# Performance work log

Hardware: AMD Instinct MI355X
Metric: run time of the kernel (lower is better)

Reference implementation:

```python
import jax, jax.numpy as jnp
import numpy as np

BATCH_SIZE = 4
TEMPERATURE = 0.07
NEG_MASK_VAL = -10.0


def setup_inputs() -> dict:
    key = jax.random.key(0)
    k1, k2 = jax.random.split(key)
    N, D = 16384, 256  # N = batch_size * n_patches
    feat_q = jax.random.normal(k1, (N, D), dtype=jnp.float32)
    feat_k = jax.random.normal(k2, (N, D), dtype=jnp.float32)
    return {"feat_q": feat_q, "feat_k": feat_k}


def reference(feat_q, feat_k):
    N, d = feat_q.shape
    feat_k = jax.lax.stop_gradient(feat_k)  # detach
    # positive logits: dot of matching rows -> [N, 1]
    l_pos = jnp.einsum('nd,nd->n', feat_q, feat_k)[:, None]
    q = feat_q.reshape(BATCH_SIZE, -1, d)  # [B, P, D]
    k = feat_k.reshape(BATCH_SIZE, -1, d)
    P = q.shape[1]
    # intra-batch-element negatives: [B, P, P]
    l_neg = jnp.einsum('bpd,bqd->bpq', q, k)
    eye = jnp.eye(P, dtype=bool)[None, :, :]
    l_neg = jnp.where(eye, jnp.float32(NEG_MASK_VAL), l_neg).reshape(-1, P)
    out = jnp.concatenate([l_pos, l_neg], axis=1) / TEMPERATURE  # [N, 1+P]
    # cross-entropy with target class 0, reduction='none'
    loss = -jax.nn.log_softmax(out, axis=1)[:, 0]
    return loss
```

## Files before the change

### kernel.cpp

```cpp
#include <hip/hip_runtime.h>
#include <hip/hip_bf16.h>


typedef __attribute__((ext_vector_type(8))) short short8;
typedef __attribute__((ext_vector_type(4))) float f32x4;

#define BATCH 4
#define PN 4096
#define DD 256
#define NP (BATCH * PN)

constexpr float kLog2e = 1.4426950408889634f;
constexpr float kScale = kLog2e / 0.07f;
constexpr float kMask2 = -10.0f * kScale;
constexpr float kLn2   = 0.6931471805599453f;
constexpr float kNegInf = -3.0e38f;

__device__ __forceinline__ unsigned short f2bf(float f) {
  __hip_bfloat16 h = __float2bfloat16(f);
  return *reinterpret_cast<unsigned short*>(&h);
}

__device__ __forceinline__ float fexp2(float x) {
#if __has_builtin(__builtin_amdgcn_exp2f)
  return __builtin_amdgcn_exp2f(x);
#else
  return exp2f(x);
#endif
}
__device__ __forceinline__ float flog2(float x) {
#if __has_builtin(__builtin_amdgcn_logf)
  return __builtin_amdgcn_logf(x);
#else
  return log2f(x);
#endif
}

__global__ void k_convert(const float* __restrict__ src,
                          unsigned short* __restrict__ dst, int n4) {
  int i = blockIdx.x * blockDim.x + threadIdx.x;
  if (i >= n4) return;
  float4 v = reinterpret_cast<const float4*>(src)[i];
  ushort4 o;
  o.x = f2bf(v.x); o.y = f2bf(v.y); o.z = f2bf(v.z); o.w = f2bf(v.w);
  reinterpret_cast<ushort4*>(dst)[i] = o;
}

__device__ __forceinline__ void stage16(const char* __restrict__ src,
                                        char* ldsbase, int tid) {
  const int wv = tid >> 6;
#pragma unroll
  for (int ip = 0; ip < 4; ip++) {
    const int o   = ip * 4096 + tid * 16;
    const int row = o >> 9;
    const int so  = o ^ ((row & 15) << 4);
    __builtin_amdgcn_global_load_lds(
        (const __attribute__((address_space(1))) void*)(src + so),
        (__attribute__((address_space(3))) void*)(ldsbase + ip * 4096 + wv * 1024),
        16, 0, 0);
  }
}

__device__ __forceinline__ void stage_tile(const char* __restrict__ src,
                                           char* ldsbase, int tid) {
  const int wv = tid >> 6;
#pragma unroll
  for (int ip = 0; ip < 8; ip++) {
    const int o   = ip * 4096 + tid * 16;
    const int row = o >> 9;
    const int so  = o ^ ((row & 15) << 4);
    __builtin_amdgcn_global_load_lds(
        (const __attribute__((address_space(1))) void*)(src + so),
        (__attribute__((address_space(3))) void*)(ldsbase + ip * 4096 + wv * 1024),
        16, 0, 0);
  }
}

__global__ __launch_bounds__(256)
__attribute__((amdgpu_waves_per_eu(2, 2)))
void k_nce256(const float* __restrict__ fq, const unsigned short* __restrict__ kb,
              float* __restrict__ pl, float* __restrict__ pp) {
  __shared__ __align__(16) char kt[2][32 * 512];

  const int blk = blockIdx.x;
  const int b   = blk & 3;
  const int r2  = blk >> 2;
  const int rt  = r2 & 15;
  const int kc  = r2 >> 4;
  const int R0  = rt * 256;
  const int C0  = kc * 512;
  const int tid = threadIdx.x;
  const int w   = tid >> 6;
  const int l   = tid & 63;
  const int g   = l >> 4;
  const int li  = l & 15;

  const char* ksrc = reinterpret_cast<const char*>(kb) +
                     ((size_t)b * PN + C0) * 512;

  stage16(ksrc, kt[0], tid);

  short8 a[4][8];
#pragma unroll
  for (int af = 0; af < 4; af++) {
    const float* qrow =
        fq + ((size_t)(b * PN + R0 + w * 64 + af * 16 + li)) * DD;
#pragma unroll
    for (int ks = 0; ks < 8; ks++) {
      const float* p = qrow + ks * 32 + g * 8;
      float4 v0 = *reinterpret_cast<const float4*>(p);
      float4 v1 = *reinterpret_cast<const float4*>(p + 4);
      a[af][ks][0] = (short)f2bf(v0.x * kScale);
      a[af][ks][1] = (short)f2bf(v0.y * kScale);
      a[af][ks][2] = (short)f2bf(v0.z * kScale);
      a[af][ks][3] = (short)f2bf(v0.w * kScale);
      a[af][ks][4] = (short)f2bf(v1.x * kScale);
      a[af][ks][5] = (short)f2bf(v1.y * kScale);
      a[af][ks][6] = (short)f2bf(v1.z * kScale);
      a[af][ks][7] = (short)f2bf(v1.w * kScale);
    }
  }

  float m[4][4], lsum[4][4];
#pragma unroll
  for (int af = 0; af < 4; af++)
#pragma unroll
    for (int r = 0; r < 4; r++) { m[af][r] = kNegInf; lsum[af][r] = 0.f; }

  __syncthreads();

  for (int ct = 0; ct < 16; ct++) {
    const int cur = ct & 1;
    if (ct + 1 < 16) stage16(ksrc + (size_t)(ct + 1) * 16384, kt[cur ^ 1], tid);

    const char* lb = kt[cur];
    f32x4 acc[4][2];
#pragma unroll
    for (int af = 0; af < 4; af++)
#pragma unroll
      for (int cf = 0; cf < 2; cf++) acc[af][cf] = f32x4{0.f, 0.f, 0.f, 0.f};

#pragma unroll
    for (int ks = 0; ks < 8; ks++) {
#pragma unroll
      for (int cf = 0; cf < 2; cf++) {
        const int row = cf * 16 + li;
        const int off = row * 512 + ((ks * 64 + g * 16) ^ ((row & 15) << 4));
        short8 bf = *reinterpret_cast<const short8*>(lb + off);
#pragma unroll
        for (int af = 0; af < 4; af++)
          acc[af][cf] = __builtin_amdgcn_mfma_f32_16x16x32_bf16(a[af][ks], bf,
                                                                acc[af][cf], 0, 0, 0);
      }
    }

#pragma unroll
    for (int af = 0; af < 4; af++) {
      const int G = rt * 16 + w * 4 + af;
      if ((G >> 5) == kc && ct == ((G >> 1) - kc * 16)) {
        if ((G & 1) == 0) {
#pragma unroll
          for (int r = 0; r < 4; r++)
            if (li == g * 4 + r) {
              pp[b * PN + R0 + w * 64 + af * 16 + g * 4 + r] = acc[af][0][r];
              acc[af][0][r] = kMask2;
            }
        } else {
#pragma unroll
          for (int r = 0; r < 4; r++)
            if (li == g * 4 + r) {
              pp[b * PN + R0 + w * 64 + af * 16 + g * 4 + r] = acc[af][1][r];
              acc[af][1][r] = kMask2;
            }
        }
      }
    }

#pragma unroll
    for (int af = 0; af < 4; af++)
#pragma unroll
      for (int r = 0; r < 4; r++) {
        float v0 = acc[af][0][r], v1 = acc[af][1][r];
        float t0 = fmaxf(v0, v1);
        float mo = m[af][r];
        float mn = fmaxf(mo, t0);
        lsum[af][r] = lsum[af][r] * fexp2(mo - mn) + fexp2(v0 - mn) + fexp2(v1 - mn);
        m[af][r] = mn;
      }
    __syncthreads();
  }

#pragma unroll
  for (int af = 0; af < 4; af++)
#pragma unroll
    for (int r = 0; r < 4; r++) {
      float m_ = m[af][r], l_ = lsum[af][r];
#pragma unroll
      for (int off = 1; off < 16; off <<= 1) {
        float mo = __shfl_xor(m_, off, 64);
        float lo = __shfl_xor(l_, off, 64);
        float mn = fmaxf(m_, mo);
        l_ = l_ * fexp2(m_ - mn) + lo * fexp2(mo - mn);
        m_ = mn;
      }
      if (li == 0) {
        const int rowg = b * PN + R0 + w * 64 + af * 16 + g * 4 + r;
        pl[kc * NP + rowg] = m_ + flog2(l_);
      }
    }
}

template <int NC>
__global__ void k_combine(const float* __restrict__ pl,
                          const float* __restrict__ pp,
                          float* __restrict__ out) {
  const int i = blockIdx.x * blockDim.x + threadIdx.x;
  if (i >= NP) return;
  float mm = kNegInf;
  float v[NC];
#pragma unroll
  for (int c = 0; c < NC; c++) { v[c] = pl[c * NP + i]; mm = fmaxf(mm, v[c]); }
  float s = 0.f;
#pragma unroll
  for (int c = 0; c < NC; c++) s += fexp2(v[c] - mm);
  float lse = mm + flog2(s);
  float p = pp[i];
  float mn = fmaxf(lse, p);
  float la = mn + flog2(fexp2(lse - mn) + fexp2(p - mn));
  out[i] = (la - p) * kLn2;
}

__global__ __launch_bounds__(256, 4) void k_nce32(
    const float* __restrict__ fq, const unsigned short* __restrict__ kb,
    float* __restrict__ pl, float* __restrict__ pp) {
  __shared__ __align__(16) char kt[2][32 * 512];

  const int blk = blockIdx.x;
  const int b   = blk & 3;
  const int rt  = (blk >> 2) & 31;
  const int kc  = blk >> 7;
  const int R0  = rt * 128;
  const int C0  = kc * 512;
  const int tid = threadIdx.x;
  const int w   = tid >> 6;
  const int l   = tid & 63;
  const int g   = l >> 4;
  const int li  = l & 15;

  const char* ksrc = reinterpret_cast<const char*>(kb) +
                     ((size_t)b * PN + C0) * 512;
  stage16(ksrc, kt[0], tid);

  short8 a[2][8];
#pragma unroll
  for (int af = 0; af < 2; af++) {
    const float* qrow = fq + ((size_t)(b * PN + R0 + w * 32 + af * 16 + li)) * DD;
#pragma unroll
    for (int ks = 0; ks < 8; ks++) {
      const float* p = qrow + ks * 32 + g * 8;
      float4 v0 = *reinterpret_cast<const float4*>(p);
      float4 v1 = *reinterpret_cast<const float4*>(p + 4);
      a[af][ks][0] = (short)f2bf(v0.x * kScale); a[af][ks][1] = (short)f2bf(v0.y * kScale);
      a[af][ks][2] = (short)f2bf(v0.z * kScale); a[af][ks][3] = (short)f2bf(v0.w * kScale);
      a[af][ks][4] = (short)f2bf(v1.x * kScale); a[af][ks][5] = (short)f2bf(v1.y * kScale);
      a[af][ks][6] = (short)f2bf(v1.z * kScale); a[af][ks][7] = (short)f2bf(v1.w * kScale);
    }
  }

  float m[2][4], lsum[2][4];
#pragma unroll
  for (int af = 0; af < 2; af++)
#pragma unroll
    for (int r = 0; r < 4; r++) { m[af][r] = kNegInf; lsum[af][r] = 0.f; }

  const int ctd = (kc == (rt >> 2)) ? ((rt & 3) * 4 + w) : -1;
  __syncthreads();

  for (int ct = 0; ct < 16; ct++) {
    const int cur = ct & 1;
    if (ct + 1 < 16) stage16(ksrc + (size_t)(ct + 1) * 16384, kt[cur ^ 1], tid);

    const char* lb = kt[cur];
    f32x4 acc[2][2];
#pragma unroll
    for (int af = 0; af < 2; af++)
#pragma unroll
      for (int cf = 0; cf < 2; cf++) acc[af][cf] = f32x4{0.f, 0.f, 0.f, 0.f};

#pragma unroll
    for (int ks = 0; ks < 8; ks++) {
#pragma unroll
      for (int cf = 0; cf < 2; cf++) {
        const int row = cf * 16 + li;
        const int off = row * 512 + ((ks * 64 + g * 16) ^ ((row & 15) << 4));
        short8 bf = *reinterpret_cast<const short8*>(lb + off);
        acc[0][cf] = __builtin_amdgcn_mfma_f32_16x16x32_bf16(a[0][ks], bf, acc[0][cf], 0, 0, 0);
        acc[1][cf] = __builtin_amdgcn_mfma_f32_16x16x32_bf16(a[1][ks], bf, acc[1][cf], 0, 0, 0);
      }
    }

    if (ct == ctd) {
#pragma unroll
      for (int af = 0; af < 2; af++)
#pragma unroll
        for (int r = 0; r < 4; r++)
          if (li == g * 4 + r) {
            pp[b * PN + R0 + w * 32 + af * 16 + g * 4 + r] = acc[af][af][r];
            acc[af][af][r] = kMask2;
          }
    }

#pragma unroll
    for (int af = 0; af < 2; af++)
#pragma unroll
      for (int r = 0; r < 4; r++) {
        float v0 = acc[af][0][r], v1 = acc[af][1][r];
        float t0 = fmaxf(v0, v1);
        float mo = m[af][r];
        float mn = fmaxf(mo, t0);
        lsum[af][r] = lsum[af][r] * fexp2(mo - mn) + fexp2(v0 - mn) + fexp2(v1 - mn);
        m[af][r] = mn;
      }
    __syncthreads();
  }

#pragma unroll
  for (int af = 0; af < 2; af++)
#pragma unroll
    for (int r = 0; r < 4; r++) {
      float m_ = m[af][r], l_ = lsum[af][r];
#pragma unroll
      for (int off = 1; off < 16; off <<= 1) {
        float mo = __shfl_xor(m_, off, 64);
        float lo = __shfl_xor(l_, off, 64);
        float mn = fmaxf(m_, mo);
        l_ = l_ * fexp2(m_ - mn) + lo * fexp2(mo - mn);
        m_ = mn;
      }
      if (li == 0) {
        const int rowg = b * PN + R0 + w * 32 + af * 16 + g * 4 + r;
        pl[kc * NP + rowg] = m_ + flog2(l_);
      }
    }
}

__global__ __launch_bounds__(256) void k_nce_full(const float* __restrict__ fq,
                                                  const unsigned short* __restrict__ kb,
                                                  float* __restrict__ out) {
  __shared__ __align__(16) char kt[2][64 * 512];
  const int blk = blockIdx.x;
  const int b = blk & 3, rt = blk >> 2;
  const int R0 = rt * 64;
  const int tid = threadIdx.x;
  const int w = tid >> 6, l = tid & 63, g = l >> 4, li = l & 15;

  const float* qrow = fq + ((size_t)(b * PN + R0 + w * 16 + li)) * DD;
  short8 a[8];
#pragma unroll
  for (int ks = 0; ks < 8; ks++) {
    const float* p = qrow + ks * 32 + g * 8;
    float4 v0 = *reinterpret_cast<const float4*>(p);
    float4 v1 = *reinterpret_cast<const float4*>(p + 4);
    a[ks][0] = (short)f2bf(v0.x * kScale); a[ks][1] = (short)f2bf(v0.y * kScale);
    a[ks][2] = (short)f2bf(v0.z * kScale); a[ks][3] = (short)f2bf(v0.w * kScale);
    a[ks][4] = (short)f2bf(v1.x * kScale); a[ks][5] = (short)f2bf(v1.y * kScale);
    a[ks][6] = (short)f2bf(v1.z * kScale); a[ks][7] = (short)f2bf(v1.w * kScale);
  }
  float m[4], lsum[4], pos[4];
#pragma unroll
  for (int r = 0; r < 4; r++) { m[r] = kNegInf; lsum[r] = 0.f; pos[r] = kNegInf; }
  const char* ksrc = reinterpret_cast<const char*>(kb + (size_t)b * PN * DD);
  stage_tile(ksrc, kt[0], tid);
  __syncthreads();
  for (int ct = 0; ct < 64; ct++) {
    const int cur = ct & 1;
    if (ct + 1 < 64) stage_tile(ksrc + (size_t)(ct + 1) * 32768, kt[cur ^ 1], tid);
    const char* lb = kt[cur];
    f32x4 acc[4];
#pragma unroll
    for (int cf = 0; cf < 4; cf++) acc[cf] = f32x4{0.f, 0.f, 0.f, 0.f};
#pragma unroll
    for (int ks = 0; ks < 8; ks++) {
#pragma unroll
      for (int cf = 0; cf < 4; cf++) {
        const int row = cf * 16 + li;
        const int off = row * 512 + ((ks * 64 + g * 16) ^ ((row & 15) << 4));
        short8 bf = *reinterpret_cast<const short8*>(lb + off);
        acc[cf] = __builtin_amdgcn_mfma_f32_16x16x32_bf16(a[ks], bf, acc[cf], 0, 0, 0);
      }
    }
    if (ct == rt) {
#pragma unroll
      for (int cf = 0; cf < 4; cf++)
        if (cf == w) {
#pragma unroll
          for (int r = 0; r < 4; r++)
            if (li == g * 4 + r) { pos[r] = acc[cf][r]; acc[cf][r] = kMask2; }
        }
    }
#pragma unroll
    for (int r = 0; r < 4; r++) {
      float t0 = fmaxf(fmaxf(acc[0][r], acc[1][r]), fmaxf(acc[2][r], acc[3][r]));
      float mo = m[r];
      float mn = fmaxf(mo, t0);
      float s = fexp2(acc[0][r] - mn) + fexp2(acc[1][r] - mn) +
                fexp2(acc[2][r] - mn) + fexp2(acc[3][r] - mn);
      lsum[r] = lsum[r] * fexp2(mo - mn) + s;
      m[r] = mn;
    }
    __syncthreads();
  }
#pragma unroll
  for (int r = 0; r < 4; r++) {
    float m_ = m[r], l_ = lsum[r], p_ = pos[r];
#pragma unroll
    for (int off = 1; off < 16; off <<= 1) {
      float mo = __shfl_xor(m_, off, 64);
      float lo = __shfl_xor(l_, off, 64);
      float po = __shfl_xor(p_, off, 64);
      float mn = fmaxf(m_, mo);
      l_ = l_ * fexp2(m_ - mn) + lo * fexp2(mo - mn);
      m_ = mn;
      p_ = fmaxf(p_, po);
    }
    float mn  = fmaxf(m_, p_);
    float lse = mn + flog2(l_ * fexp2(m_ - mn) + fexp2(p_ - mn));
    if (li == 0) out[b * PN + R0 + w * 16 + g * 4 + r] = (lse - p_) * kLn2;
  }
}

extern "C" void kernel_launch(void* const* d_in, const int* in_sizes, int n_in,
                              void* d_out, int out_size, void* d_ws, size_t ws_size,
                              hipStream_t stream) {
  const float* fq = (const float*)d_in[0];
  const float* fk = (const float*)d_in[1];
  float* out = (float*)d_out;
  unsigned short* kb = (unsigned short*)d_ws;
  const size_t kbBytes = (size_t)NP * DD * 2;
  const size_t ppBytes = (size_t)NP * 4;
  const size_t pl8Bytes = (size_t)8 * NP * 4;

  const int n4 = (NP * DD) / 4;
  hipLaunchKernelGGL(k_convert, dim3(n4 / 256), dim3(256), 0, stream, fk, kb, n4);

  if (ws_size >= kbBytes + pl8Bytes + ppBytes) {
    float* pl = (float*)((char*)d_ws + kbBytes);
    float* pp = (float*)((char*)d_ws + kbBytes + pl8Bytes);
    hipLaunchKernelGGL(k_nce256, dim3(512), dim3(256), 0, stream, fq, kb, pl, pp);
    hipLaunchKernelGGL(k_combine<8>, dim3(NP / 256), dim3(256), 0, stream, pl, pp, out);
  } else {
    hipLaunchKernelGGL(k_nce_full, dim3(BATCH * (PN / 64)), dim3(256), 0, stream,
                       fq, kb, out);
  }
}
```

Baseline: 63.50 us.

## Pre-convert Q to scaled bf16 and use smaller 128-row tiles with higher occupancy

A combined conversion kernel now turns both Q (pre-scaled) and K into bf16 in one launch. The main kernel becomes k_nceQ: 128-row tiles over 1024 blocks with 4 waves per EU, and it loads bf16 Q fragments directly instead of converting fp32 in registers. This removes the per-block fp32 Q reads and conversion, and aims for more parallelism and occupancy. In exchange it needs extra workspace and write traffic for the Q buffer, and each K tile is reused by fewer query rows.

```diff
diff --git a/kernel.cpp b/kernel.cpp
--- a/kernel.cpp
+++ b/kernel.cpp
@@ -34,6 +34,27 @@
 #else
   return log2f(x);
 #endif
+}
+
+__global__ void k_convert2(const float* __restrict__ fq,
+                           const float* __restrict__ fk,
+                           unsigned short* __restrict__ qb,
+                           unsigned short* __restrict__ kb, int n4each) {
+  int i = blockIdx.x * blockDim.x + threadIdx.x;
+  if (i < n4each) {
+    float4 v = reinterpret_cast<const float4*>(fq)[i];
+    ushort4 o;
+    o.x = f2bf(v.x * kScale); o.y = f2bf(v.y * kScale);
+    o.z = f2bf(v.z * kScale); o.w = f2bf(v.w * kScale);
+    reinterpret_cast<ushort4*>(qb)[i] = o;
+  } else {
+    int j = i - n4each;
+    if (j >= n4each) return;
+    float4 v = reinterpret_cast<const float4*>(fk)[j];
+    ushort4 o;
+    o.x = f2bf(v.x); o.y = f2bf(v.y); o.z = f2bf(v.z); o.w = f2bf(v.w);
+    reinterpret_cast<ushort4*>(kb)[j] = o;
+  }
 }
 
 __global__ void k_convert(const float* __restrict__ src,
@@ -77,162 +98,10 @@
 }
 
 __global__ __launch_bounds__(256)
-__attribute__((amdgpu_waves_per_eu(2, 2)))
-void k_nce256(const float* __restrict__ fq, const unsigned short* __restrict__ kb,
-              float* __restrict__ pl, float* __restrict__ pp) {
-  __shared__ __align__(16) char kt[2][32 * 512];
-
-  const int blk = blockIdx.x;
-  const int b   = blk & 3;
-  const int r2  = blk >> 2;
-  const int rt  = r2 & 15;
-  const int kc  = r2 >> 4;
-  const int R0  = rt * 256;
-  const int C0  = kc * 512;
-  const int tid = threadIdx.x;
-  const int w   = tid >> 6;
-  const int l   = tid & 63;
-  const int g   = l >> 4;
-  const int li  = l & 15;
-
-  const char* ksrc = reinterpret_cast<const char*>(kb) +
-                     ((size_t)b * PN + C0) * 512;
-
-  stage16(ksrc, kt[0], tid);
-
-  short8 a[4][8];
-#pragma unroll
-  for (int af = 0; af < 4; af++) {
-    const float* qrow =
-        fq + ((size_t)(b * PN + R0 + w * 64 + af * 16 + li)) * DD;
-#pragma unroll
-    for (int ks = 0; ks < 8; ks++) {
-      const float* p = qrow + ks * 32 + g * 8;
-      float4 v0 = *reinterpret_cast<const float4*>(p);
-      float4 v1 = *reinterpret_cast<const float4*>(p + 4);
-      a[af][ks][0] = (short)f2bf(v0.x * kScale);
-      a[af][ks][1] = (short)f2bf(v0.y * kScale);
-      a[af][ks][2] = (short)f2bf(v0.z * kScale);
-      a[af][ks][3] = (short)f2bf(v0.w * kScale);
-      a[af][ks][4] = (short)f2bf(v1.x * kScale);
-      a[af][ks][5] = (short)f2bf(v1.y * kScale);
-      a[af][ks][6] = (short)f2bf(v1.z * kScale);
-      a[af][ks][7] = (short)f2bf(v1.w * kScale);
-    }
-  }
-
-  float m[4][4], lsum[4][4];
-#pragma unroll
-  for (int af = 0; af < 4; af++)
-#pragma unroll
-    for (int r = 0; r < 4; r++) { m[af][r] = kNegInf; lsum[af][r] = 0.f; }
-
-  __syncthreads();
-
-  for (int ct = 0; ct < 16; ct++) {
-    const int cur = ct & 1;
-    if (ct + 1 < 16) stage16(ksrc + (size_t)(ct + 1) * 16384, kt[cur ^ 1], tid);
-
-    const char* lb = kt[cur];
-    f32x4 acc[4][2];
-#pragma unroll
-    for (int af = 0; af < 4; af++)
-#pragma unroll
-      for (int cf = 0; cf < 2; cf++) acc[af][cf] = f32x4{0.f, 0.f, 0.f, 0.f};
-
-#pragma unroll
-    for (int ks = 0; ks < 8; ks++) {
-#pragma unroll
-      for (int cf = 0; cf < 2; cf++) {
-        const int row = cf * 16 + li;
-        const int off = row * 512 + ((ks * 64 + g * 16) ^ ((row & 15) << 4));
-        short8 bf = *reinterpret_cast<const short8*>(lb + off);
-#pragma unroll
-        for (int af = 0; af < 4; af++)
-          acc[af][cf] = __builtin_amdgcn_mfma_f32_16x16x32_bf16(a[af][ks], bf,
-                                                                acc[af][cf], 0, 0, 0);
-      }
-    }
-
-#pragma unroll
-    for (int af = 0; af < 4; af++) {
-      const int G = rt * 16 + w * 4 + af;
-      if ((G >> 5) == kc && ct == ((G >> 1) - kc * 16)) {
-        if ((G & 1) == 0) {
-#pragma unroll
-          for (int r = 0; r < 4; r++)
-            if (li == g * 4 + r) {
-              pp[b * PN + R0 + w * 64 + af * 16 + g * 4 + r] = acc[af][0][r];
-              acc[af][0][r] = kMask2;
-            }
-        } else {
-#pragma unroll
-          for (int r = 0; r < 4; r++)
-            if (li == g * 4 + r) {
-              pp[b * PN + R0 + w * 64 + af * 16 + g * 4 + r] = acc[af][1][r];
-              acc[af][1][r] = kMask2;
-            }
-        }
-      }
-    }
-
-#pragma unroll
-    for (int af = 0; af < 4; af++)
-#pragma unroll
-      for (int r = 0; r < 4; r++) {
-        float v0 = acc[af][0][r], v1 = acc[af][1][r];
-        float t0 = fmaxf(v0, v1);
-        float mo = m[af][r];
-        float mn = fmaxf(mo, t0);
-        lsum[af][r] = lsum[af][r] * fexp2(mo - mn) + fexp2(v0 - mn) + fexp2(v1 - mn);
-        m[af][r] = mn;
-      }
-    __syncthreads();
-  }
-
-#pragma unroll
-  for (int af = 0; af < 4; af++)
-#pragma unroll
-    for (int r = 0; r < 4; r++) {
-      float m_ = m[af][r], l_ = lsum[af][r];
-#pragma unroll
-      for (int off = 1; off < 16; off <<= 1) {
-        float mo = __shfl_xor(m_, off, 64);
-        float lo = __shfl_xor(l_, off, 64);
-        float mn = fmaxf(m_, mo);
-        l_ = l_ * fexp2(m_ - mn) + lo * fexp2(mo - mn);
-        m_ = mn;
-      }
-      if (li == 0) {
-        const int rowg = b * PN + R0 + w * 64 + af * 16 + g * 4 + r;
-        pl[kc * NP + rowg] = m_ + flog2(l_);
-      }
-    }
-}
-
-template <int NC>
-__global__ void k_combine(const float* __restrict__ pl,
-                          const float* __restrict__ pp,
-                          float* __restrict__ out) {
-  const int i = blockIdx.x * blockDim.x + threadIdx.x;
-  if (i >= NP) return;
-  float mm = kNegInf;
-  float v[NC];
-#pragma unroll
-  for (int c = 0; c < NC; c++) { v[c] = pl[c * NP + i]; mm = fmaxf(mm, v[c]); }
-  float s = 0.f;
-#pragma unroll
-  for (int c = 0; c < NC; c++) s += fexp2(v[c] - mm);
-  float lse = mm + flog2(s);
-  float p = pp[i];
-  float mn = fmaxf(lse, p);
-  float la = mn + flog2(fexp2(lse - mn) + fexp2(p - mn));
-  out[i] = (la - p) * kLn2;
-}
-
-__global__ __launch_bounds__(256, 4) void k_nce32(
-    const float* __restrict__ fq, const unsigned short* __restrict__ kb,
-    float* __restrict__ pl, float* __restrict__ pp) {
+__attribute__((amdgpu_waves_per_eu(4, 4)))
+void k_nceQ(const unsigned short* __restrict__ qb,
+            const unsigned short* __restrict__ kb,
+            float* __restrict__ pl, float* __restrict__ pp) {
   __shared__ __align__(16) char kt[2][32 * 512];
 
   const int blk = blockIdx.x;
@@ -249,6 +118,143 @@
 
   const char* ksrc = reinterpret_cast<const char*>(kb) +
                      ((size_t)b * PN + C0) * 512;
+
+  stage16(ksrc, kt[0], tid);
+
+  short8 a[2][8];
+#pragma unroll
+  for (int af = 0; af < 2; af++) {
+    const unsigned short* qrow =
+        qb + (size_t)(b * PN + R0 + w * 32 + af * 16 + li) * DD;
+#pragma unroll
+    for (int ks = 0; ks < 8; ks++)
+      a[af][ks] = *reinterpret_cast<const short8*>(qrow + ks * 32 + g * 8);
+  }
+#pragma unroll
+  for (int af = 0; af < 2; af++)
+#pragma unroll
+    for (int ks = 0; ks < 8; ks++)
+      asm volatile("" : "+v"(a[af][ks]));
+
+  float m[2][4], lsum[2][4];
+#pragma unroll
+  for (int af = 0; af < 2; af++)
+#pragma unroll
+    for (int r = 0; r < 4; r++) { m[af][r] = kNegInf; lsum[af][r] = 0.f; }
+
+  const int ctd = (kc == (rt >> 2)) ? ((rt & 3) * 4 + w) : -1;
+
+  __syncthreads();
+
+  for (int ct = 0; ct < 16; ct++) {
+    const int cur = ct & 1;
+    if (ct + 1 < 16) stage16(ksrc + (size_t)(ct + 1) * 16384, kt[cur ^ 1], tid);
+
+    const char* lb = kt[cur];
+    f32x4 acc[2][2];
+#pragma unroll
+    for (int af = 0; af < 2; af++)
+#pragma unroll
+      for (int cf = 0; cf < 2; cf++) acc[af][cf] = f32x4{0.f, 0.f, 0.f, 0.f};
+
+#pragma unroll
+    for (int ks = 0; ks < 8; ks++) {
+#pragma unroll
+      for (int cf = 0; cf < 2; cf++) {
+        const int row = cf * 16 + li;
+        const int off = row * 512 + ((ks * 64 + g * 16) ^ ((row & 15) << 4));
+        short8 bf = *reinterpret_cast<const short8*>(lb + off);
+        acc[0][cf] = __builtin_amdgcn_mfma_f32_16x16x32_bf16(a[0][ks], bf,
+                                                             acc[0][cf], 0, 0, 0);
+        acc[1][cf] = __builtin_amdgcn_mfma_f32_16x16x32_bf16(a[1][ks], bf,
+                                                             acc[1][cf], 0, 0, 0);
+      }
+    }
+
+    if (ct == ctd) {
+#pragma unroll
+      for (int af = 0; af < 2; af++)
+#pragma unroll
+        for (int r = 0; r < 4; r++)
+          if (li == g * 4 + r) {
+            pp[b * PN + R0 + w * 32 + af * 16 + g * 4 + r] = acc[af][af][r];
+            acc[af][af][r] = kMask2;
+          }
+    }
+
+#pragma unroll
+    for (int af = 0; af < 2; af++)
+#pragma unroll
+      for (int r = 0; r < 4; r++) {
+        float v0 = acc[af][0][r], v1 = acc[af][1][r];
+        float t0 = fmaxf(v0, v1);
+        float mo = m[af][r];
+        float mn = fmaxf(mo, t0);
+        lsum[af][r] = lsum[af][r] * fexp2(mo - mn) + fexp2(v0 - mn) + fexp2(v1 - mn);
+        m[af][r] = mn;
+      }
+    __syncthreads();
+  }
+
+#pragma unroll
+  for (int af = 0; af < 2; af++)
+#pragma unroll
+    for (int r = 0; r < 4; r++) {
+      float m_ = m[af][r], l_ = lsum[af][r];
+#pragma unroll
+      for (int off = 1; off < 16; off <<= 1) {
+        float mo = __shfl_xor(m_, off, 64);
+        float lo = __shfl_xor(l_, off, 64);
+        float mn = fmaxf(m_, mo);
+        l_ = l_ * fexp2(m_ - mn) + lo * fexp2(mo - mn);
+        m_ = mn;
+      }
+      if (li == 0) {
+        const int rowg = b * PN + R0 + w * 32 + af * 16 + g * 4 + r;
+        pl[kc * NP + rowg] = m_ + flog2(l_);
+      }
+    }
+}
+
+template <int NC>
+__global__ void k_combine(const float* __restrict__ pl,
+                          const float* __restrict__ pp,
+                          float* __restrict__ out) {
+  const int i = blockIdx.x * blockDim.x + threadIdx.x;
+  if (i >= NP) return;
+  float mm = kNegInf;
+  float v[NC];
+#pragma unroll
+  for (int c = 0; c < NC; c++) { v[c] = pl[c * NP + i]; mm = fmaxf(mm, v[c]); }
+  float s = 0.f;
+#pragma unroll
+  for (int c = 0; c < NC; c++) s += fexp2(v[c] - mm);
+  float lse = mm + flog2(s);
+  float p = pp[i];
+  float mn = fmaxf(lse, p);
+  float la = mn + flog2(fexp2(lse - mn) + fexp2(p - mn));
+  out[i] = (la - p) * kLn2;
+}
+
+__global__ __launch_bounds__(256, 4) void k_nce32(
+    const float* __restrict__ fq, const unsigned short* __restrict__ kb,
+    float* __restrict__ pl, float* __restrict__ pp) {
+  __shared__ __align__(16) char kt[2][32 * 512];
+
+  const int blk = blockIdx.x;
+  const int b   = blk & 3;
+  const int rt  = (blk >> 2) & 31;
+  const int kc  = blk >> 7;
+  const int R0  = rt * 128;
+  const int C0  = kc * 512;
+  const int tid = threadIdx.x;
+  const int w   = tid >> 6;
+  const int l   = tid & 63;
+  const int g   = l >> 4;
+  const int li  = l & 15;
+
+  const char* ksrc = reinterpret_cast<const char*>(kb) +
+                     ((size_t)b * PN + C0) * 512;
   stage16(ksrc, kt[0], tid);
 
   short8 a[2][8];
@@ -435,20 +441,30 @@
   const float* fq = (const float*)d_in[0];
   const float* fk = (const float*)d_in[1];
   float* out = (float*)d_out;
-  unsigned short* kb = (unsigned short*)d_ws;
-  const size_t kbBytes = (size_t)NP * DD * 2;
-  const size_t ppBytes = (size_t)NP * 4;
+  const size_t bufBytes = (size_t)NP * DD * 2;
+  const size_t ppBytes  = (size_t)NP * 4;
   const size_t pl8Bytes = (size_t)8 * NP * 4;
-
-  const int n4 = (NP * DD) / 4;
-  hipLaunchKernelGGL(k_convert, dim3(n4 / 256), dim3(256), 0, stream, fk, kb, n4);
-
-  if (ws_size >= kbBytes + pl8Bytes + ppBytes) {
-    float* pl = (float*)((char*)d_ws + kbBytes);
-    float* pp = (float*)((char*)d_ws + kbBytes + pl8Bytes);
-    hipLaunchKernelGGL(k_nce256, dim3(512), dim3(256), 0, stream, fq, kb, pl, pp);
+  const int n4each = (NP * DD) / 4;
+
+  if (ws_size >= 2 * bufBytes + pl8Bytes + ppBytes) {
+    unsigned short* qb = (unsigned short*)d_ws;
+    unsigned short* kb = (unsigned short*)((char*)d_ws + bufBytes);
+    float* pl = (float*)((char*)d_ws + 2 * bufBytes);
+    float* pp = (float*)((char*)d_ws + 2 * bufBytes + pl8Bytes);
+    hipLaunchKernelGGL(k_convert2, dim3((2 * n4each) / 256), dim3(256), 0, stream,
+                       fq, fk, qb, kb, n4each);
+    hipLaunchKernelGGL(k_nceQ, dim3(1024), dim3(256), 0, stream, qb, kb, pl, pp);
+    hipLaunchKernelGGL(k_combine<8>, dim3(NP / 256), dim3(256), 0, stream, pl, pp, out);
+  } else if (ws_size >= bufBytes + pl8Bytes + ppBytes) {
+    unsigned short* kb = (unsigned short*)d_ws;
+    float* pl = (float*)((char*)d_ws + bufBytes);
+    float* pp = (float*)((char*)d_ws + bufBytes + pl8Bytes);
+    hipLaunchKernelGGL(k_convert, dim3(n4each / 256), dim3(256), 0, stream, fk, kb, n4each);
+    hipLaunchKernelGGL(k_nce32, dim3(1024), dim3(256), 0, stream, fq, kb, pl, pp);
     hipLaunchKernelGGL(k_combine<8>, dim3(NP / 256), dim3(256), 0, stream, pl, pp, out);
   } else {
+    unsigned short* kb = (unsigned short*)d_ws;
+    hipLaunchKernelGGL(k_convert, dim3(n4each / 256), dim3(256), 0, stream, fk, kb, n4each);
     hipLaunchKernelGGL(k_nce_full, dim3(BATCH * (PN / 64)), dim3(256), 0, stream,
                        fq, kb, out);
   }
```

Measured after the change: 58.69 us. 7.6% less time.
